# Performance work log

Measured on AMD Instinct MI355X. Metric: run time of the kernel, lower is better.

## Reference

```python
import jax, jax.numpy as jnp
import numpy as np

N = 200000          # nodes
E = 800000          # edges (avg degree ~4, molecular graphs)
F_IN = 128          # dataset.num_node_features
HID = 32            # hidden_channels -> widths 32, 64, 128
N_TASKS = 128       # dataset.num_tasks
G = 8000            # number of graphs in the batch
EPS = 1e-5


def _glorot(key, shape):
    fan_in, fan_out = shape[0], shape[1]
    lim = np.sqrt(6.0 / (fan_in + fan_out)).astype(np.float32)
    return jax.random.uniform(key, shape, jnp.float32, -lim, lim)


def setup_inputs() -> dict:
    key = jax.random.key(0)
    ks = jax.random.split(key, 16)
    x = jax.random.normal(ks[0], (N, F_IN), jnp.float32)
    edge_index = jax.random.randint(ks[1], (2, E), 0, N, jnp.int64)
    batch = jnp.sort(jax.random.randint(ks[2], (N,), 0, G, jnp.int64))
    return {
        "x": x,
        "edge_index": edge_index,
        "batch": batch,
        "norm_w": jnp.ones((1,), jnp.float32),
        "norm_b": jnp.zeros((1,), jnp.float32),
        "W1": _glorot(ks[3], (F_IN, HID)),
        "b1": jnp.zeros((HID,), jnp.float32),
        "W2": _glorot(ks[4], (HID, 2 * HID)),
        "b2": jnp.zeros((2 * HID,), jnp.float32),
        "W3": _glorot(ks[5], (2 * HID, 4 * HID)),
        "b3": jnp.zeros((4 * HID,), jnp.float32),
        "lin1_W": _glorot(ks[6], (4 * HID, 256)),
        "lin1_b": jnp.zeros((256,), jnp.float32),
        "lin2_W": _glorot(ks[7], (256, N_TASKS)),
        "lin2_b": jnp.zeros((N_TASKS,), jnp.float32),
    }


def _instance_norm(x, batch, w, b):
    # PyG InstanceNorm: per-graph, per-channel mean / biased var, scalar affine.
    ones = jnp.ones((x.shape[0], 1), x.dtype)
    cnt = jnp.maximum(jax.ops.segment_sum(ones, batch, num_segments=G), 1.0)  # [G,1]
    mean = jax.ops.segment_sum(x, batch, num_segments=G) / cnt               # [G,C]
    var = jax.ops.segment_sum(x * x, batch, num_segments=G) / cnt - mean * mean
    xn = (x - mean[batch]) * jax.lax.rsqrt(var[batch] + EPS)
    return xn * w + b


def _gcn_conv(x, src, dst, dis, W, b):
    # GCNConv: h = xW; out_i = sum_j (d_i d_j)^{-1/2} h_j over A+I edges; + bias.
    h = x @ W
    msg = h[src] * (dis[src] * dis[dst])[:, None]          # [E, C] gather
    agg = jax.ops.segment_sum(msg, dst, num_segments=x.shape[0])
    agg = agg + h * (dis * dis)[:, None]                   # self-loop term
    return agg + b


def reference(x, edge_index, batch, norm_w, norm_b, W1, b1, W2, b2, W3, b3,
              lin1_W, lin1_b, lin2_W, lin2_b):
    src, dst = edge_index[0], edge_index[1]
    # degrees on A + I (all edge weights 1)
    deg = 1.0 + jax.ops.segment_sum(jnp.ones((E,), x.dtype), dst, num_segments=N)
    dis = jax.lax.rsqrt(deg)                                # deg >= 1, safe

    h = _instance_norm(x, batch, norm_w, norm_b)
    h = jax.nn.relu(_gcn_conv(h, src, dst, dis, W1, b1))
    h = jax.nn.relu(_gcn_conv(h, src, dst, dis, W2, b2))
    h = jax.nn.relu(_gcn_conv(h, src, dst, dis, W3, b3))

    # global_max_pool; empty graphs -> 0 (values are >=0 post-relu)
    pooled = jnp.maximum(jax.ops.segment_max(h, batch, num_segments=G), 0.0)

    out = jax.nn.relu(pooled @ lin1_W + lin1_b)
    return out @ lin2_W + lin2_b
```

## Files before the change

kernel.cpp:

```cpp
#include <hip/hip_runtime.h>
#include <hip/hip_bf16.h>
#include <stdint.h>

#define NN 200000
#define NE 800000
#define FIN 128
#define NG 8000
#define EPSV 1e-5f
#define NBS ((NN + 255) / 256)
#define CNT_B (NE / 256)

typedef __attribute__((ext_vector_type(8))) short bf16x8;
typedef __attribute__((ext_vector_type(4))) float f32x4;

static __device__ __forceinline__ bf16x8 as_bf16x8(uint4 u) {
    union { uint4 u; bf16x8 v; } c; c.u = u; return c.v;
}

static __device__ __forceinline__ void u2f(uint4 v, float4& lo, float4& hi) {
    lo.x = __uint_as_float(v.x << 16); lo.y = __uint_as_float(v.x & 0xffff0000u);
    lo.z = __uint_as_float(v.y << 16); lo.w = __uint_as_float(v.y & 0xffff0000u);
    hi.x = __uint_as_float(v.z << 16); hi.y = __uint_as_float(v.z & 0xffff0000u);
    hi.z = __uint_as_float(v.w << 16); hi.w = __uint_as_float(v.w & 0xffff0000u);
}
static __device__ __forceinline__ unsigned int pk(float a, float b) {
    __hip_bfloat16 x = __float2bfloat16(a), y = __float2bfloat16(b);
    return (unsigned int)(*(unsigned short*)&x) | ((unsigned int)(*(unsigned short*)&y) << 16);
}

__global__ __launch_bounds__(256) void k_prep1(const int* __restrict__ dst, int* __restrict__ cnt,
                                               const int* __restrict__ batch, int* __restrict__ startg,
                                               const float* __restrict__ W3,
                                               unsigned short* __restrict__ whi,
                                               unsigned short* __restrict__ wlo) {
    int b = blockIdx.x, t = threadIdx.x;
    if (b < CNT_B) {
        int e = b * 256 + t;
        atomicAdd(&cnt[dst[e]], 1);
    } else if (b < CNT_B + NBS) {
        int n = (b - CNT_B) * 256 + t;
        if (n >= NN) return;
        int bb = batch[n];
        int prev = (n == 0) ? -1 : batch[n - 1];
        for (int g = prev + 1; g <= bb; ++g) startg[g] = n;
        if (n == NN - 1) {
            for (int g = bb + 1; g <= NG; ++g) startg[g] = NN;
        }
    } else {
        int i = (b - CNT_B - NBS) * 256 + t;
        if (i >= 64 * 128) return;
        int n = i >> 6, k = i & 63;
        float w = W3[k * 128 + n];
        __hip_bfloat16 h = __float2bfloat16(w);
        float hf = __bfloat162float(h);
        __hip_bfloat16 l = __float2bfloat16(w - hf);
        whi[n * 64 + k] = *(unsigned short*)&h;
        wlo[n * 64 + k] = *(unsigned short*)&l;
    }
}

__global__ void k_blocksum(const int* __restrict__ cnt, int* __restrict__ bsum) {
    __shared__ int sh[256];
    int b = blockIdx.x, t = threadIdx.x;
    int idx = b * 256 + t;
    sh[t] = (idx < NN) ? cnt[idx] : 0;
    __syncthreads();
    for (int o = 128; o > 0; o >>= 1) {
        if (t < o) sh[t] += sh[t + o];
        __syncthreads();
    }
    if (t == 0) bsum[b] = sh[0];
}

__global__ __launch_bounds__(1024) void k_scanb(const int* __restrict__ bsum, int* __restrict__ bpre) {
    __shared__ int sh[1024];
    int t = threadIdx.x;
    int v = (t < NBS) ? bsum[t] : 0;
    sh[t] = v;
    __syncthreads();
    for (int o = 1; o < 1024; o <<= 1) {
        int add = (t >= o) ? sh[t - o] : 0;
        __syncthreads();
        sh[t] += add;
        __syncthreads();
    }
    if (t < NBS) bpre[t] = sh[t] - v;
}

__global__ void k_scanchunk(int* __restrict__ cnt, const int* __restrict__ bpre,
                            int* __restrict__ rowstart, int* __restrict__ cursor) {
    __shared__ int sh[256];
    int b = blockIdx.x, t = threadIdx.x;
    int idx = b * 256 + t;
    int v = (idx < NN) ? cnt[idx] : 0;
    sh[t] = v;
    __syncthreads();
    for (int o = 1; o < 256; o <<= 1) {
        int add = (t >= o) ? sh[t - o] : 0;
        __syncthreads();
        sh[t] += add;
        __syncthreads();
    }
    if (idx < NN) {
        int rs = bpre[b] + sh[t] - v;
        rowstart[idx] = rs;
        cursor[idx] = rs;
        ((float*)cnt)[idx] = rsqrtf(1.0f + (float)v);
    }
    if (idx == 0) rowstart[NN] = NE;
}

__global__ void k_fill(const int* __restrict__ src, const int* __restrict__ dst,
                       int* __restrict__ cursor, int* __restrict__ csr) {
    int e = blockIdx.x * 256 + threadIdx.x;
    if (e < NE) {
        int pos = atomicAdd(&cursor[dst[e]], 1);
        csr[pos] = src[e];
    }
}

__global__ __launch_bounds__(256) void k_stats2(const float* __restrict__ x,
                                                const int* __restrict__ startg,
                                                const float* __restrict__ nw,
                                                const float* __restrict__ nb,
                                                float* __restrict__ scale,
                                                float* __restrict__ shift) {
    __shared__ float4 rsum[256], rsq[256];
    int g = blockIdx.x;
    int s = startg[g], e = startg[g + 1];
    if (s == e) return;
    int t = threadIdx.x;
    int slot = t >> 5, c4 = t & 31;
    const float4* x4 = (const float4*)x;
    float4 sum = {0.f, 0.f, 0.f, 0.f}, sq = {0.f, 0.f, 0.f, 0.f};
    for (int n = s + slot; n < e; n += 8) {
        float4 v = x4[n * 32 + c4];
        sum.x += v.x; sum.y += v.y; sum.z += v.z; sum.w += v.w;
        sq.x += v.x * v.x; sq.y += v.y * v.y; sq.z += v.z * v.z; sq.w += v.w * v.w;
    }
    rsum[slot * 32 + c4] = sum;
    rsq[slot * 32 + c4] = sq;
    __syncthreads();
    if (t < 32) {
        float4 S = rsum[t], Q = rsq[t];
#pragma unroll
        for (int sl = 1; sl < 8; ++sl) {
            float4 a = rsum[sl * 32 + t], bq = rsq[sl * 32 + t];
            S.x += a.x; S.y += a.y; S.z += a.z; S.w += a.w;
            Q.x += bq.x; Q.y += bq.y; Q.z += bq.z; Q.w += bq.w;
        }
        float inv = 1.0f / (float)(e - s);
        float w = nw[0], bb = nb[0];
        float4 sc, sh;
        {
            float m = S.x * inv, v = fmaxf(Q.x * inv - m * m, 0.f);
            float is = rsqrtf(v + EPSV); sc.x = is * w; sh.x = bb - m * is * w;
        }
        {
            float m = S.y * inv, v = fmaxf(Q.y * inv - m * m, 0.f);
            float is = rsqrtf(v + EPSV); sc.y = is * w; sh.y = bb - m * is * w;
        }
        {
            float m = S.z * inv, v = fmaxf(Q.z * inv - m * m, 0.f);
            float is = rsqrtf(v + EPSV); sc.z = is * w; sh.z = bb - m * is * w;
        }
        {
            float m = S.w * inv, v = fmaxf(Q.w * inv - m * m, 0.f);
            float is = rsqrtf(v + EPSV); sc.w = is * w; sh.w = bb - m * is * w;
        }
        ((float4*)scale)[g * 32 + t] = sc;
        ((float4*)shift)[g * 32 + t] = sh;
    }
}

__global__ __launch_bounds__(256) void k_conv1s(const float* __restrict__ x,
                                                const int* __restrict__ batch,
                                                const float* __restrict__ scale,
                                                const float* __restrict__ shift,
                                                const float* __restrict__ W1,
                                                const float* __restrict__ dis,
                                                float* __restrict__ p1) {
    __shared__ float4 sx4[64 * 33];
    int t = threadIdx.x;
    int base = blockIdx.x * 64;
    const float4* x4 = (const float4*)x;
    const float4* sc4 = (const float4*)scale;
    const float4* sh4 = (const float4*)shift;
    for (int i = t; i < 64 * 32; i += 256) {
        int nl = i >> 5, c4 = i & 31;
        int n = base + nl;
        int g = batch[n];
        float4 xv = x4[n * 32 + c4];
        float4 sc = sc4[g * 32 + c4];
        float4 sh = sh4[g * 32 + c4];
        float4 r;
        r.x = fmaf(xv.x, sc.x, sh.x);
        r.y = fmaf(xv.y, sc.y, sh.y);
        r.z = fmaf(xv.z, sc.z, sh.z);
        r.w = fmaf(xv.w, sc.w, sh.w);
        sx4[nl * 33 + c4] = r;
    }
    __syncthreads();
    int lane = t & 63;
    int kq = __builtin_amdgcn_readfirstlane(t >> 6) * 2;
    const float4* W4 = (const float4*)W1;
    const float4* arow = &sx4[lane * 33];
    float4 acc0 = {0.f, 0.f, 0.f, 0.f}, acc1 = {0.f, 0.f, 0.f, 0.f};
#pragma unroll 4
    for (int c4 = 0; c4 < 32; ++c4) {
        float4 a = arow[c4];
        int rb = c4 * 32 + kq;
        float4 wA0 = W4[rb +  0], wA1 = W4[rb +  1];
        float4 wB0 = W4[rb +  8], wB1 = W4[rb +  9];
        float4 wC0 = W4[rb + 16], wC1 = W4[rb + 17];
        float4 wD0 = W4[rb + 24], wD1 = W4[rb + 25];
        acc0.x += a.x * wA0.x + a.y * wB0.x + a.z * wC0.x + a.w * wD0.x;
        acc0.y += a.x * wA0.y + a.y * wB0.y + a.z * wC0.y + a.w * wD0.y;
        acc0.z += a.x * wA0.z + a.y * wB0.z + a.z * wC0.z + a.w * wD0.z;
        acc0.w += a.x * wA0.w + a.y * wB0.w + a.z * wC0.w + a.w * wD0.w;
        acc1.x += a.x * wA1.x + a.y * wB1.x + a.z * wC1.x + a.w * wD1.x;
        acc1.y += a.x * wA1.y + a.y * wB1.y + a.z * wC1.y + a.w * wD1.y;
        acc1.z += a.x * wA1.z + a.y * wB1.z + a.z * wC1.z + a.w * wD1.z;
        acc1.w += a.x * wA1.w + a.y * wB1.w + a.z * wC1.w + a.w * wD1.w;
    }
    int n = base + lane;
    float d = dis[n];
    float4 r0, r1;
    r0.x = acc0.x * d; r0.y = acc0.y * d; r0.z = acc0.z * d; r0.w = acc0.w * d;
    r1.x = acc1.x * d; r1.y = acc1.y * d; r1.z = acc1.z * d; r1.w = acc1.w * d;
    ((float4*)p1)[n * 8 + kq] = r0;
    ((float4*)p1)[n * 8 + kq + 1] = r1;
}

__global__ __launch_bounds__(256) void k_gather1(const float* __restrict__ p1,
                                                 const int* __restrict__ rowstart,
                                                 const int* __restrict__ csr,
                                                 const float* __restrict__ dis,
                                                 const float* __restrict__ b1,
                                                 float* __restrict__ p2) {
    int tid = blockIdx.x * 256 + threadIdx.x;
    int n = tid >> 3, c4 = tid & 7;
    const float4* p1_4 = (const float4*)p1;
    int s = rowstart[n], e = rowstart[n + 1];
    float4 agg = p1_4[n * 8 + c4];
    int j = s;
    for (; j + 1 < e; j += 2) {
        float4 v0 = p1_4[csr[j] * 8 + c4];
        float4 v1 = p1_4[csr[j + 1] * 8 + c4];
        agg.x += v0.x + v1.x; agg.y += v0.y + v1.y;
        agg.z += v0.z + v1.z; agg.w += v0.w + v1.w;
    }
    if (j < e) {
        float4 v = p1_4[csr[j] * 8 + c4];
        agg.x += v.x; agg.y += v.y; agg.z += v.z; agg.w += v.w;
    }
    float d = dis[n];
    float4 bb = ((const float4*)b1)[c4];
    float4 r;
    r.x = fmaxf(d * agg.x + bb.x, 0.f) * d;
    r.y = fmaxf(d * agg.y + bb.y, 0.f) * d;
    r.z = fmaxf(d * agg.z + bb.z, 0.f) * d;
    r.w = fmaxf(d * agg.w + bb.w, 0.f) * d;
    ((float4*)p2)[n * 8 + c4] = r;
}

__global__ __launch_bounds__(256) void k_conv2g(const float* __restrict__ p2,
                                                const int* __restrict__ rowstart,
                                                const int* __restrict__ csr,
                                                const float* __restrict__ dis,
                                                const float* __restrict__ W2,
                                                const float* __restrict__ b2v,
                                                __hip_bfloat16* __restrict__ p3h) {
    __shared__ float sW[32 * 64];
    __shared__ float4 spart[16 * 16];
    __shared__ float sa[16 * 32];
    int t = threadIdx.x;
    const float4* W4 = (const float4*)W2;
    for (int i = t; i < 32 * 64 / 4; i += 256) ((float4*)sW)[i] = W4[i];
    int base = blockIdx.x * 16;
    const float4* p2_4 = (const float4*)p2;
    {
        int node = t >> 4, c4 = t & 7, half = (t >> 3) & 1;
        int n = base + node;
        int s = rowstart[n], e = rowstart[n + 1];
        float4 agg = {0.f, 0.f, 0.f, 0.f};
        if (half == 0) {
            agg = p2_4[n * 8 + c4];
            for (int j = s; j < e; j += 2) {
                float4 v = p2_4[csr[j] * 8 + c4];
                agg.x += v.x; agg.y += v.y; agg.z += v.z; agg.w += v.w;
            }
        } else {
            for (int j = s + 1; j < e; j += 2) {
                float4 v = p2_4[csr[j] * 8 + c4];
                agg.x += v.x; agg.y += v.y; agg.z += v.z; agg.w += v.w;
            }
        }
        spart[node * 16 + half * 8 + c4] = agg;
    }
    __syncthreads();
    if (t < 128) {
        int nd = t >> 3, cc = t & 7;
        float4 a = spart[nd * 16 + cc], b = spart[nd * 16 + 8 + cc];
        float d = dis[base + nd];
        float4 r;
        r.x = d * (a.x + b.x); r.y = d * (a.y + b.y);
        r.z = d * (a.z + b.z); r.w = d * (a.w + b.w);
        ((float4*)sa)[nd * 8 + cc] = r;
    }
    __syncthreads();
    int k = t & 63, grp = t >> 6;
    float acc[4] = {0.f, 0.f, 0.f, 0.f};
    for (int c = 0; c < 32; ++c) {
        float w = sW[c * 64 + k];
#pragma unroll
        for (int q = 0; q < 4; ++q) acc[q] += sa[(grp * 4 + q) * 32 + c] * w;
    }
    float bb = b2v[k];
#pragma unroll
    for (int q = 0; q < 4; ++q) {
        int n = base + grp * 4 + q;
        float h = fmaxf(acc[q] + bb, 0.f);
        p3h[n * 64 + k] = __float2bfloat16(h * dis[n]);
    }
}

__global__ __launch_bounds__(256) void k_conv3mg(const __hip_bfloat16* __restrict__ p3h,
                                                 const int* __restrict__ rowstart,
                                                 const int* __restrict__ csr,
                                                 const float* __restrict__ dis,
                                                 const unsigned short* __restrict__ w3hi,
                                                 const unsigned short* __restrict__ w3lo,
                                                 const float* __restrict__ b3v,
                                                 const int* __restrict__ batch,
                                                 unsigned int* __restrict__ pooled) {
    __shared__ uint4 sa[64 * 9];
    __shared__ int sbatch[64];
    int t = threadIdx.x;
    int base = blockIdx.x * 64;
    if (t < 64) sbatch[t] = batch[base + t];
    const uint4* p3q = (const uint4*)p3h;
    for (int i = t; i < 64 * 8; i += 256) {
        int nl = i >> 3, c8 = i & 7;
        int n = base + nl;
        int s = rowstart[n], e = rowstart[n + 1];
        float4 alo, ahi;
        u2f(p3q[n * 8 + c8], alo, ahi);
        int j = s;
        for (; j + 1 < e; j += 2) {
            float4 l0, h0, l1, h1;
            u2f(p3q[csr[j] * 8 + c8], l0, h0);
            u2f(p3q[csr[j + 1] * 8 + c8], l1, h1);
            alo.x += l0.x + l1.x; alo.y += l0.y + l1.y;
            alo.z += l0.z + l1.z; alo.w += l0.w + l1.w;
            ahi.x += h0.x + h1.x; ahi.y += h0.y + h1.y;
            ahi.z += h0.z + h1.z; ahi.w += h0.w + h1.w;
        }
        if (j < e) {
            float4 l0, h0;
            u2f(p3q[csr[j] * 8 + c8], l0, h0);
            alo.x += l0.x; alo.y += l0.y; alo.z += l0.z; alo.w += l0.w;
            ahi.x += h0.x; ahi.y += h0.y; ahi.z += h0.z; ahi.w += h0.w;
        }
        float d = dis[n];
        uint4 o;
        o.x = pk(d * alo.x, d * alo.y);
        o.y = pk(d * alo.z, d * alo.w);
        o.z = pk(d * ahi.x, d * ahi.y);
        o.w = pk(d * ahi.z, d * ahi.w);
        sa[nl * 9 + c8] = o;
    }
    __syncthreads();
    int lane = t & 63, w = t >> 6;
    int h = lane >> 4;
    int cid = lane & 15;
    const uint4* WHq = (const uint4*)w3hi;
    const uint4* WLq = (const uint4*)w3lo;
    uint4 bh[2][2], bl[2][2];
#pragma unroll
    for (int nl = 0; nl < 2; ++nl) {
        int n = (w * 2 + nl) * 16 + cid;
#pragma unroll
        for (int kt = 0; kt < 2; ++kt) {
            bh[nl][kt] = WHq[n * 8 + kt * 4 + h];
            bl[nl][kt] = WLq[n * 8 + kt * 4 + h];
        }
    }
    f32x4 acc[2][4];
#pragma unroll
    for (int nl = 0; nl < 2; ++nl)
#pragma unroll
        for (int mi = 0; mi < 4; ++mi) acc[nl][mi] = {0.f, 0.f, 0.f, 0.f};
#pragma unroll
    for (int mi = 0; mi < 4; ++mi) {
        int arow = (mi * 16 + cid) * 9;
        bf16x8 a0 = as_bf16x8(sa[arow + h]);
        bf16x8 a1 = as_bf16x8(sa[arow + 4 + h]);
#pragma unroll
        for (int nl = 0; nl < 2; ++nl) {
            acc[nl][mi] = __builtin_amdgcn_mfma_f32_16x16x32_bf16(a0, as_bf16x8(bh[nl][0]), acc[nl][mi], 0, 0, 0);
            acc[nl][mi] = __builtin_amdgcn_mfma_f32_16x16x32_bf16(a1, as_bf16x8(bh[nl][1]), acc[nl][mi], 0, 0, 0);
            acc[nl][mi] = __builtin_amdgcn_mfma_f32_16x16x32_bf16(a0, as_bf16x8(bl[nl][0]), acc[nl][mi], 0, 0, 0);
            acc[nl][mi] = __builtin_amdgcn_mfma_f32_16x16x32_bf16(a1, as_bf16x8(bl[nl][1]), acc[nl][mi], 0, 0, 0);
        }
    }
    __syncthreads();
    unsigned int* spool = (unsigned int*)sa;
    for (int i = t; i < 16 * 128; i += 256) spool[i] = 0u;
    __syncthreads();
    int g0 = sbatch[0], g63 = sbatch[63];
    int ch0 = (w * 2) * 16 + cid, ch1 = ch0 + 16;
    float bb0 = b3v[ch0], bb1 = b3v[ch1];
    int curg = sbatch[h * 4];
    float cm0 = 0.f, cm1 = 0.f;
#pragma unroll
    for (int mi = 0; mi < 4; ++mi) {
#pragma unroll
        for (int r = 0; r < 4; ++r) {
            int node_l = mi * 16 + h * 4 + r;
            int g = sbatch[node_l];
            if (g != curg) {
                int s = curg - g0 - 1;
                if (s >= 0 && curg < g63 && s < 16) {
                    atomicMax(&spool[s * 128 + ch0], __float_as_uint(cm0));
                    atomicMax(&spool[s * 128 + ch1], __float_as_uint(cm1));
                } else {
                    atomicMax(&pooled[curg * 128 + ch0], __float_as_uint(cm0));
                    atomicMax(&pooled[curg * 128 + ch1], __float_as_uint(cm1));
                }
                cm0 = 0.f; cm1 = 0.f;
                curg = g;
            }
            cm0 = fmaxf(cm0, fmaxf(acc[0][mi][r] + bb0, 0.f));
            cm1 = fmaxf(cm1, fmaxf(acc[1][mi][r] + bb1, 0.f));
        }
    }
    {
        int s = curg - g0 - 1;
        if (s >= 0 && curg < g63 && s < 16) {
            atomicMax(&spool[s * 128 + ch0], __float_as_uint(cm0));
            atomicMax(&spool[s * 128 + ch1], __float_as_uint(cm1));
        } else {
            atomicMax(&pooled[curg * 128 + ch0], __float_as_uint(cm0));
            atomicMax(&pooled[curg * 128 + ch1], __float_as_uint(cm1));
        }
    }
    __syncthreads();
    {
        int s = t >> 4;
        int g = g0 + 1 + s;
        if (g < g63) {
            int ch = (t & 15) * 8;
            const float* spf = (const float*)spool;
            float4 v0 = *(const float4*)&spf[s * 128 + ch];
            float4 v1 = *(const float4*)&spf[s * 128 + ch + 4];
            float4* pf = (float4*)pooled;
            pf[g * 32 + (ch >> 2)] = v0;
            pf[g * 32 + (ch >> 2) + 1] = v1;
        }
    }
}

__global__ __launch_bounds__(256) void k_head(const float* __restrict__ pooled,
                                              const float* __restrict__ W1v,
                                              const float* __restrict__ b1v,
                                              const float* __restrict__ W2v,
                                              const float* __restrict__ b2v,
                                              float* __restrict__ out) {
    __shared__ __align__(16) float sp[8 * 128];
    __shared__ __align__(16) float smid[8 * 256];
    __shared__ __align__(16) float sred[8 * 128];
    int t = threadIdx.x;
    int base = blockIdx.x * 8;
    const float4* po4 = (const float4*)pooled;
    for (int i = t; i < 8 * 32; i += 256) ((float4*)sp)[i] = po4[base * 32 + i];
    __syncthreads();
    {
        float acc[8];
#pragma unroll
        for (int gl = 0; gl < 8; ++gl) acc[gl] = 0.f;
        const float4* sp4 = (const float4*)sp;
        for (int c4 = 0; c4 < 32; ++c4) {
            float w0 = W1v[(c4 * 4 + 0) * 256 + t];
            float w1 = W1v[(c4 * 4 + 1) * 256 + t];
            float w2 = W1v[(c4 * 4 + 2) * 256 + t];
            float w3 = W1v[(c4 * 4 + 3) * 256 + t];
#pragma unroll
            for (int gl = 0; gl < 8; ++gl) {
                float4 a = sp4[gl * 32 + c4];
                acc[gl] += a.x * w0 + a.y * w1 + a.z * w2 + a.w * w3;
            }
        }
        float bb = b1v[t];
#pragma unroll
        for (int gl = 0; gl < 8; ++gl) smid[gl * 256 + t] = fmaxf(acc[gl] + bb, 0.f);
    }
    __syncthreads();
    int k = t & 127, half = t >> 7;
    float acc2[8];
#pragma unroll
    for (int gl = 0; gl < 8; ++gl) acc2[gl] = 0.f;
    {
        const float* Wc = W2v + half * 128 * 128;
        const float4* sm4 = (const float4*)smid;
        for (int c4 = 0; c4 < 32; ++c4) {
            float w0 = Wc[(c4 * 4 + 0) * 128 + k];
            float w1 = Wc[(c4 * 4 + 1) * 128 + k];
            float w2 = Wc[(c4 * 4 + 2) * 128 + k];
            float w3 = Wc[(c4 * 4 + 3) * 128 + k];
#pragma unroll
            for (int gl = 0; gl < 8; ++gl) {
                float4 a = sm4[gl * 64 + half * 32 + c4];
                acc2[gl] += a.x * w0 + a.y * w1 + a.z * w2 + a.w * w3;
            }
        }
    }
    if (half == 1) {
#pragma unroll
        for (int gl = 0; gl < 8; ++gl) sred[gl * 128 + k] = acc2[gl];
    }
    __syncthreads();
    if (half == 0) {
        float bb = b2v[k];
#pragma unroll
        for (int gl = 0; gl < 8; ++gl)
            out[(base + gl) * 128 + k] = acc2[gl] + sred[gl * 128 + k] + bb;
    }
}

extern "C" void kernel_launch(void* const* d_in, const int* in_sizes, int n_in,
                              void* d_out, int out_size, void* d_ws, size_t ws_size,
                              hipStream_t stream) {
    (void)in_sizes; (void)n_in; (void)out_size; (void)ws_size;
    const float* x   = (const float*)d_in[0];
    const int* ei    = (const int*)d_in[1];
    const int* src = ei;
    const int* dst = ei + NE;
    const int* batch = (const int*)d_in[2];
    const float* nw  = (const float*)d_in[3];
    const float* nb  = (const float*)d_in[4];
    const float* W1  = (const float*)d_in[5];
    const float* b1  = (const float*)d_in[6];
    const float* W2  = (const float*)d_in[7];
    const float* b2  = (const float*)d_in[8];
    const float* W3  = (const float*)d_in[9];
    const float* b3  = (const float*)d_in[10];
    const float* l1W = (const float*)d_in[11];
    const float* l1b = (const float*)d_in[12];
    const float* l2W = (const float*)d_in[13];
    const float* l2b = (const float*)d_in[14];
    float* out = (float*)d_out;

    char* wsp = (char*)d_ws;
    int*   cnt      = (int*)wsp;   wsp += (size_t)NN * 4;
    int*   rowstart = (int*)wsp;   wsp += (size_t)(NN + 1) * 4;
    int*   cursor   = (int*)wsp;   wsp += (size_t)NN * 4;
    int*   bsum     = (int*)wsp;   wsp += (size_t)NBS * 4;
    int*   bpre     = (int*)wsp;   wsp += (size_t)NBS * 4;
    int*   startg   = (int*)wsp;   wsp += (size_t)(NG + 1) * 4;
    int*   csr      = (int*)wsp;   wsp += (size_t)NE * 4;
    wsp += ((256 - ((uintptr_t)wsp & 255)) & 255);
    unsigned short* w3hi = (unsigned short*)wsp; wsp += (size_t)128 * 64 * 2;
    unsigned short* w3lo = (unsigned short*)wsp; wsp += (size_t)128 * 64 * 2;
    float* scale   = (float*)wsp; wsp += (size_t)NG * 128 * 4;
    float* shift   = (float*)wsp; wsp += (size_t)NG * 128 * 4;
    float* pooled  = (float*)wsp; wsp += (size_t)NG * 128 * 4;
    float* regionA = (float*)wsp; wsp += (size_t)NN * 64 * 4;
    float* regionB = (float*)wsp; wsp += (size_t)NN * 64 * 4;

    float* dis  = (float*)cnt;
    float* p1   = regionA;
    float* p2   = regionA + (size_t)NN * 32;
    __hip_bfloat16* p3h = (__hip_bfloat16*)regionB;

    hipMemsetAsync(cnt, 0, (size_t)NN * 4, stream);
    k_prep1<<<CNT_B + NBS + 32, 256, 0, stream>>>(dst, cnt, batch, startg, W3, w3hi, w3lo);
    k_blocksum<<<NBS, 256, 0, stream>>>(cnt, bsum);
    k_scanb<<<1, 1024, 0, stream>>>(bsum, bpre);
    k_scanchunk<<<NBS, 256, 0, stream>>>(cnt, bpre, rowstart, cursor);
    k_fill<<<(NE + 255) / 256, 256, 0, stream>>>(src, dst, cursor, csr);

    k_stats2<<<NG, 256, 0, stream>>>(x, startg, nw, nb, scale, shift);
    k_conv1s<<<NN / 64, 256, 0, stream>>>(x, batch, scale, shift, W1, dis, p1);
    k_gather1<<<NN * 8 / 256, 256, 0, stream>>>(p1, rowstart, csr, dis, b1, p2);
    k_conv2g<<<NN / 16, 256, 0, stream>>>(p2, rowstart, csr, dis, W2, b2, p3h);
    hipMemsetAsync(pooled, 0, (size_t)NG * 128 * 4, stream);
    k_conv3mg<<<NN / 64, 256, 0, stream>>>(p3h, rowstart, csr, dis, w3hi, w3lo, b3, batch,
                                           (unsigned int*)pooled);

    k_head<<<NG / 8, 256, 0, stream>>>(pooled, l1W, l1b, l2W, l2b, out);
}
```

Measured before the change: 474.9 us.

## Use split-bf16 MFMA for conv2 transform with 64-node tiles

Replaces the scalar FP32 32x64 matmul in the second GCN layer with bf16 MFMA 16x16x32 instructions. It uses a hi/lo split of both activations and weights (four MFMAs) to keep near-FP32 accuracy. W2 is pre-split into transposed bf16 hi/lo arrays inside the prep kernel. The tile grows from 16 to 64 nodes per block, with each thread gathering full neighbor rows itself instead of two half-threads per row. This removes shared-memory FP32 FMA loops and a sync stage, but reduces the number of blocks and adds split/pack overhead.

New measurement: 449.2 us. 5.4% less time.

```diff
diff --git a/kernel.cpp b/kernel.cpp
--- a/kernel.cpp
+++ b/kernel.cpp
@@ -27,12 +27,20 @@
     __hip_bfloat16 x = __float2bfloat16(a), y = __float2bfloat16(b);
     return (unsigned int)(*(unsigned short*)&x) | ((unsigned int)(*(unsigned short*)&y) << 16);
 }
+static __device__ __forceinline__ void spl(float v, float& hf, float& lf) {
+    __hip_bfloat16 h = __float2bfloat16(v);
+    hf = __bfloat162float(h);
+    lf = v - hf;
+}
 
 __global__ __launch_bounds__(256) void k_prep1(const int* __restrict__ dst, int* __restrict__ cnt,
                                                const int* __restrict__ batch, int* __restrict__ startg,
                                                const float* __restrict__ W3,
-                                               unsigned short* __restrict__ whi,
-                                               unsigned short* __restrict__ wlo) {
+                                               unsigned short* __restrict__ w3hi,
+                                               unsigned short* __restrict__ w3lo,
+                                               const float* __restrict__ W2,
+                                               unsigned short* __restrict__ w2hi,
+                                               unsigned short* __restrict__ w2lo) {
     int b = blockIdx.x, t = threadIdx.x;
     if (b < CNT_B) {
         int e = b * 256 + t;
@@ -46,7 +54,7 @@
         if (n == NN - 1) {
             for (int g = bb + 1; g <= NG; ++g) startg[g] = NN;
         }
-    } else {
+    } else if (b < CNT_B + NBS + 32) {
         int i = (b - CNT_B - NBS) * 256 + t;
         if (i >= 64 * 128) return;
         int n = i >> 6, k = i & 63;
@@ -54,8 +62,18 @@
         __hip_bfloat16 h = __float2bfloat16(w);
         float hf = __bfloat162float(h);
         __hip_bfloat16 l = __float2bfloat16(w - hf);
-        whi[n * 64 + k] = *(unsigned short*)&h;
-        wlo[n * 64 + k] = *(unsigned short*)&l;
+        w3hi[n * 64 + k] = *(unsigned short*)&h;
+        w3lo[n * 64 + k] = *(unsigned short*)&l;
+    } else {
+        int i = (b - CNT_B - NBS - 32) * 256 + t;
+        if (i >= 64 * 32) return;
+        int ch = i >> 5, k = i & 31;
+        float w = W2[k * 64 + ch];
+        __hip_bfloat16 h = __float2bfloat16(w);
+        float hf = __bfloat162float(h);
+        __hip_bfloat16 l = __float2bfloat16(w - hf);
+        w2hi[ch * 32 + k] = *(unsigned short*)&h;
+        w2lo[ch * 32 + k] = *(unsigned short*)&l;
     }
 }
 
@@ -264,64 +282,80 @@
     ((float4*)p2)[n * 8 + c4] = r;
 }
 
-__global__ __launch_bounds__(256) void k_conv2g(const float* __restrict__ p2,
+__global__ __launch_bounds__(256) void k_conv2m(const float* __restrict__ p2,
                                                 const int* __restrict__ rowstart,
                                                 const int* __restrict__ csr,
                                                 const float* __restrict__ dis,
-                                                const float* __restrict__ W2,
+                                                const unsigned short* __restrict__ w2hi,
+                                                const unsigned short* __restrict__ w2lo,
                                                 const float* __restrict__ b2v,
                                                 __hip_bfloat16* __restrict__ p3h) {
-    __shared__ float sW[32 * 64];
-    __shared__ float4 spart[16 * 16];
-    __shared__ float sa[16 * 32];
+    __shared__ uint2 sah[64 * 10];
+    __shared__ uint2 sal[64 * 10];
+    __shared__ float sdis[64];
     int t = threadIdx.x;
-    const float4* W4 = (const float4*)W2;
-    for (int i = t; i < 32 * 64 / 4; i += 256) ((float4*)sW)[i] = W4[i];
-    int base = blockIdx.x * 16;
+    int base = blockIdx.x * 64;
+    if (t < 64) sdis[t] = dis[base + t];
     const float4* p2_4 = (const float4*)p2;
-    {
-        int node = t >> 4, c4 = t & 7, half = (t >> 3) & 1;
-        int n = base + node;
+    for (int i = t; i < 64 * 8; i += 256) {
+        int nl = i >> 3, c4 = i & 7;
+        int n = base + nl;
         int s = rowstart[n], e = rowstart[n + 1];
-        float4 agg = {0.f, 0.f, 0.f, 0.f};
-        if (half == 0) {
-            agg = p2_4[n * 8 + c4];
-            for (int j = s; j < e; j += 2) {
-                float4 v = p2_4[csr[j] * 8 + c4];
-                agg.x += v.x; agg.y += v.y; agg.z += v.z; agg.w += v.w;
-            }
-        } else {
-            for (int j = s + 1; j < e; j += 2) {
-                float4 v = p2_4[csr[j] * 8 + c4];
-                agg.x += v.x; agg.y += v.y; agg.z += v.z; agg.w += v.w;
-            }
-        }
-        spart[node * 16 + half * 8 + c4] = agg;
-    }
-    __syncthreads();
-    if (t < 128) {
-        int nd = t >> 3, cc = t & 7;
-        float4 a = spart[nd * 16 + cc], b = spart[nd * 16 + 8 + cc];
-        float d = dis[base + nd];
-        float4 r;
-        r.x = d * (a.x + b.x); r.y = d * (a.y + b.y);
-        r.z = d * (a.z + b.z); r.w = d * (a.w + b.w);
-        ((float4*)sa)[nd * 8 + cc] = r;
-    }
-    __syncthreads();
-    int k = t & 63, grp = t >> 6;
-    float acc[4] = {0.f, 0.f, 0.f, 0.f};
-    for (int c = 0; c < 32; ++c) {
-        float w = sW[c * 64 + k];
-#pragma unroll
-        for (int q = 0; q < 4; ++q) acc[q] += sa[(grp * 4 + q) * 32 + c] * w;
-    }
-    float bb = b2v[k];
-#pragma unroll
-    for (int q = 0; q < 4; ++q) {
-        int n = base + grp * 4 + q;
-        float h = fmaxf(acc[q] + bb, 0.f);
-        p3h[n * 64 + k] = __float2bfloat16(h * dis[n]);
+        float4 agg = p2_4[n * 8 + c4];
+        int j = s;
+        for (; j + 1 < e; j += 2) {
+            float4 v0 = p2_4[csr[j] * 8 + c4];
+            float4 v1 = p2_4[csr[j + 1] * 8 + c4];
+            agg.x += v0.x + v1.x; agg.y += v0.y + v1.y;
+            agg.z += v0.z + v1.z; agg.w += v0.w + v1.w;
+        }
+        if (j < e) {
+            float4 v = p2_4[csr[j] * 8 + c4];
+            agg.x += v.x; agg.y += v.y; agg.z += v.z; agg.w += v.w;
+        }
+        float d = dis[n];
+        float ax = d * agg.x, ay = d * agg.y, az = d * agg.z, aw = d * agg.w;
+        float hx, lx, hy, ly, hz, lz, hw, lw;
+        spl(ax, hx, lx); spl(ay, hy, ly); spl(az, hz, lz); spl(aw, hw, lw);
+        uint2 hh, ll;
+        hh.x = pk(hx, hy); hh.y = pk(hz, hw);
+        ll.x = pk(lx, ly); ll.y = pk(lz, lw);
+        sah[nl * 10 + c4] = hh;
+        sal[nl * 10 + c4] = ll;
+    }
+    __syncthreads();
+    int lane = t & 63, w = t >> 6;
+    int h = lane >> 4;
+    int cid = lane & 15;
+    int ch = w * 16 + cid;
+    const uint4* WHq = (const uint4*)w2hi;
+    const uint4* WLq = (const uint4*)w2lo;
+    bf16x8 bh = as_bf16x8(WHq[ch * 4 + h]);
+    bf16x8 bl = as_bf16x8(WLq[ch * 4 + h]);
+    const uint4* sah4 = (const uint4*)sah;
+    const uint4* sal4 = (const uint4*)sal;
+    f32x4 acc[4];
+#pragma unroll
+    for (int mi = 0; mi < 4; ++mi) acc[mi] = {0.f, 0.f, 0.f, 0.f};
+#pragma unroll
+    for (int mi = 0; mi < 4; ++mi) {
+        int arow = (mi * 16 + cid) * 5 + h;
+        bf16x8 ah = as_bf16x8(sah4[arow]);
+        bf16x8 al = as_bf16x8(sal4[arow]);
+        acc[mi] = __builtin_amdgcn_mfma_f32_16x16x32_bf16(ah, bh, acc[mi], 0, 0, 0);
+        acc[mi] = __builtin_amdgcn_mfma_f32_16x16x32_bf16(ah, bl, acc[mi], 0, 0, 0);
+        acc[mi] = __builtin_amdgcn_mfma_f32_16x16x32_bf16(al, bh, acc[mi], 0, 0, 0);
+        acc[mi] = __builtin_amdgcn_mfma_f32_16x16x32_bf16(al, bl, acc[mi], 0, 0, 0);
+    }
+    float bb = b2v[ch];
+#pragma unroll
+    for (int mi = 0; mi < 4; ++mi) {
+#pragma unroll
+        for (int r = 0; r < 4; ++r) {
+            int nloc = mi * 16 + h * 4 + r;
+            float hv = fmaxf(acc[mi][r] + bb, 0.f);
+            p3h[(size_t)(base + nloc) * 64 + ch] = __float2bfloat16(hv * sdis[nloc]);
+        }
     }
 }
 
@@ -562,6 +596,8 @@
     wsp += ((256 - ((uintptr_t)wsp & 255)) & 255);
     unsigned short* w3hi = (unsigned short*)wsp; wsp += (size_t)128 * 64 * 2;
     unsigned short* w3lo = (unsigned short*)wsp; wsp += (size_t)128 * 64 * 2;
+    unsigned short* w2hi = (unsigned short*)wsp; wsp += (size_t)64 * 32 * 2;
+    unsigned short* w2lo = (unsigned short*)wsp; wsp += (size_t)64 * 32 * 2;
     float* scale   = (float*)wsp; wsp += (size_t)NG * 128 * 4;
     float* shift   = (float*)wsp; wsp += (size_t)NG * 128 * 4;
     float* pooled  = (float*)wsp; wsp += (size_t)NG * 128 * 4;
@@ -574,7 +610,8 @@
     __hip_bfloat16* p3h = (__hip_bfloat16*)regionB;
 
     hipMemsetAsync(cnt, 0, (size_t)NN * 4, stream);
-    k_prep1<<<CNT_B + NBS + 32, 256, 0, stream>>>(dst, cnt, batch, startg, W3, w3hi, w3lo);
+    k_prep1<<<CNT_B + NBS + 40, 256, 0, stream>>>(dst, cnt, batch, startg,
+                                                  W3, w3hi, w3lo, W2, w2hi, w2lo);
     k_blocksum<<<NBS, 256, 0, stream>>>(cnt, bsum);
     k_scanb<<<1, 1024, 0, stream>>>(bsum, bpre);
     k_scanchunk<<<NBS, 256, 0, stream>>>(cnt, bpre, rowstart, cursor);
@@ -583,7 +620,7 @@
     k_stats2<<<NG, 256, 0, stream>>>(x, startg, nw, nb, scale, shift);
     k_conv1s<<<NN / 64, 256, 0, stream>>>(x, batch, scale, shift, W1, dis, p1);
     k_gather1<<<NN * 8 / 256, 256, 0, stream>>>(p1, rowstart, csr, dis, b1, p2);
-    k_conv2g<<<NN / 16, 256, 0, stream>>>(p2, rowstart, csr, dis, W2, b2, p3h);
+    k_conv2m<<<NN / 64, 256, 0, stream>>>(p2, rowstart, csr, dis, w2hi, w2lo, b2, p3h);
     hipMemsetAsync(pooled, 0, (size_t)NG * 128 * 4, stream);
     k_conv3mg<<<NN / 64, 256, 0, stream>>>(p3h, rowstart, csr, dis, w3hi, w3lo, b3, batch,
                                            (unsigned int*)pooled);
```
